# Kernel tuning notes

Measured on AMD Instinct MI355X. Metric: run time of the kernel, lower is better.

The kernel has to match this reference:

```python
import jax, jax.numpy as jnp
import numpy as np

N = 100000          # instances in the bag
L_IN = 784          # 28*28
C = 128             # size[1]
H = 2               # n_heads = len(temperature)
S = C // H          # step = 64
D = S // 2          # per-head hidden dim ('small') = 32
TEMP = jnp.array([1.0, 1.0], dtype=jnp.float32)  # temperature per head


def setup_inputs() -> dict:
    key = jax.random.key(0)
    ks = jax.random.split(key, 8)
    h = jax.random.normal(ks[0], (N, L_IN), dtype=jnp.float32)
    # shared FC: Linear(784, 128) (xavier-normal-ish init, zero bias)
    W0 = jax.random.normal(ks[1], (L_IN, C), dtype=jnp.float32) * (2.0 / (L_IN + C)) ** 0.5
    b0 = jnp.zeros((C,), dtype=jnp.float32)
    # per-head gated attention nets, stacked over head axis
    Wa = jax.random.normal(ks[2], (H, S, D), dtype=jnp.float32) * (2.0 / (S + D)) ** 0.5
    ba = jnp.zeros((H, D), dtype=jnp.float32)
    Wb = jax.random.normal(ks[3], (H, S, D), dtype=jnp.float32) * (2.0 / (S + D)) ** 0.5
    bb = jnp.zeros((H, D), dtype=jnp.float32)
    Wc = jax.random.normal(ks[4], (H, D, 1), dtype=jnp.float32) * (2.0 / (D + 1)) ** 0.5
    bc = jnp.zeros((H, 1), dtype=jnp.float32)
    # bag-level classifier: Linear(128, 1)
    Wcls = jax.random.normal(ks[5], (C, 1), dtype=jnp.float32) * (2.0 / (C + 1)) ** 0.5
    bcls = jnp.zeros((1,), dtype=jnp.float32)
    return {"h": h, "W0": W0, "b0": b0, "Wa": Wa, "ba": ba,
            "Wb": Wb, "bb": bb, "Wc": Wc, "bc": bc,
            "Wcls": Wcls, "bcls": bcls}


def reference(h, W0, b0, Wa, ba, Wb, bb, Wc, bc, Wcls, bcls):
    # shared FC + ReLU: [N,784] -> [N,128]
    x = jax.nn.relu(h @ W0 + b0)
    x = x.reshape(-1, H, S)                                  # [N,H,S]
    # gated attention per head, batched over heads via einsum
    a = jnp.tanh(jnp.einsum('nhs,hsd->nhd', x, Wa) + ba)     # [N,H,D]
    g = jax.nn.sigmoid(jnp.einsum('nhs,hsd->nhd', x, Wb) + bb)
    A = (jnp.einsum('nhd,hdo->nho', a * g, Wc) + bc)[..., 0] # [N,H]
    A = A / TEMP                                             # temperature scaling per head
    Aw = jax.nn.softmax(A, axis=0)                           # softmax over instances N
    # weighted instance pooling: [1, H*S] = [1, 128]
    M = jnp.einsum('nh,nhs->hs', Aw, x).reshape(1, H * S)
    logits = (M @ Wcls + bcls)[:, 0]                         # [1]
    Y_prob = jax.nn.sigmoid(logits)
    Y_hat = (Y_prob >= 0.5).astype(jnp.float32)
    return (Y_prob, Y_hat)
```

## Files before the change

kernel.cpp:

```cpp
#include <hip/hip_runtime.h>
#include <stdint.h>
#include <math.h>

typedef unsigned short u16;
typedef unsigned int   u32;
typedef __bf16 bf16x8 __attribute__((ext_vector_type(8)));
typedef float  f32x4  __attribute__((ext_vector_type(4)));

#define L_IN 784
#define KPAD 832
#define KT_N 13

__device__ __forceinline__ u32 f2bf(float f){
    u32 u = __float_as_uint(f);
    return (u + 0x7fffu + ((u >> 16) & 1u)) >> 16;
}

__device__ __forceinline__ void gload16(const void* g, void* l){
    __builtin_amdgcn_global_load_lds(
        (const __attribute__((address_space(1))) unsigned char*)g,
        (__attribute__((address_space(3))) unsigned char*)l, 16, 0, 0);
}

__global__ void prep_w0(const float* __restrict__ W0, u16* __restrict__ Bimg){
    int idx = blockIdx.x * 256 + threadIdx.x;
    if (idx >= KPAD * 128) return;
    int j  = idx & 7;
    int l  = (idx >> 3) & 63;
    int nt = (idx >> 9) & 7;
    int kk = (idx >> 12) & 1;
    int kt = idx >> 13;
    int col = nt * 16 + (l & 15);
    int k   = kt * 64 + kk * 32 + (l >> 4) * 8 + j;
    float v = (k < L_IN) ? W0[k * 128 + col] : 0.f;
    Bimg[idx] = (u16)f2bf(v);
}

__global__ void prep_wab(const float* __restrict__ Wa, const float* __restrict__ Wb,
                         u16* __restrict__ Wab){
    int idx = blockIdx.x * 256 + threadIdx.x;
    if (idx >= 16384) return;
    int jj  = idx & 7;
    int l   = (idx >> 3) & 63;
    int ks  = (idx >> 9) & 1;
    int nt  = (idx >> 10) & 1;
    int h   = (idx >> 11) & 1;
    int mat = (idx >> 12) & 1;
    int s = ks * 32 + (l >> 4) * 8 + jj;
    int d = nt * 16 + (l & 15);
    const float* W = mat ? Wb : Wa;
    Wab[idx] = (u16)f2bf(W[h * 2048 + s * 32 + d]);
}

__global__ __launch_bounds__(256, 4)
void fc_fused(const float* __restrict__ hG, const u16* __restrict__ Bimg,
              const u16* __restrict__ Wab, const float* __restrict__ b0,
              const float* __restrict__ ba, const float* __restrict__ bb,
              const float* __restrict__ Wc, const float* __restrict__ bc,
              float* __restrict__ partials, int N){
    __shared__ __align__(16) float As[2][64 * 64];

    const int t    = threadIdx.x;
    const int lane = t & 63;
    const int w    = t >> 6;
    const int lr   = lane & 15;
    const int lk   = lane >> 4;
    const int gb   = blockIdx.x;
    const long rowBase = (long)gb * 64;

    const int rloc = t >> 4;
    const int csw  = (t & 15) ^ ((rloc & 3) << 1);
    const float* srcp[4];
    #pragma unroll
    for (int j = 0; j < 4; ++j){
        long grow = rowBase + j * 16 + rloc;
        if (grow >= N) grow = N - 1;
        srcp[j] = hG + grow * L_IN + csw * 4;
    }

    f32x4 acc[8];
    #pragma unroll
    for (int nt = 0; nt < 8; ++nt) acc[nt] = (f32x4)0.f;

    auto stage = [&](int kt, int buf){
        #pragma unroll
        for (int j = 0; j < 4; ++j){
            const float* src = (kt == KT_N - 1 && csw >= 4)
                             ? (srcp[j] - csw * 4)
                             : (srcp[j] + kt * 64);
            gload16(src, (char*)&As[buf][0] + (j * 256 + t) * 16);
        }
    };

    stage(0, 0);
    int cur = 0;
    const int rA = w * 16 + lr;

    #pragma unroll 1
    for (int kt = 0; kt < KT_N; ++kt){
        __syncthreads();

        const u16* bp = Bimg + (size_t)(kt * 2) * 4096 + lane * 8;
        bf16x8 b0f[8], b1f[8];
        #pragma unroll
        for (int nt = 0; nt < 8; ++nt)
            b0f[nt] = *(const bf16x8*)(bp + nt * 512);
        #pragma unroll
        for (int nt = 0; nt < 8; ++nt)
            b1f[nt] = *(const bf16x8*)(bp + 4096 + nt * 512);
        __builtin_amdgcn_sched_barrier(0);

        if (kt + 1 < KT_N) stage(kt + 1, cur ^ 1);
        __builtin_amdgcn_sched_barrier(0);

        #pragma unroll
        for (int kk = 0; kk < 2; ++kk){
            const int q = kk * 4 + (lk ^ (rA & 3));
            f32x4 lo = *(const f32x4*)&As[cur][rA * 64 + q * 8];
            f32x4 hi = *(const f32x4*)&As[cur][rA * 64 + q * 8 + 4];
            bf16x8 af;
            #pragma unroll
            for (int j = 0; j < 4; ++j){
                af[j]     = (__bf16)lo[j];
                af[4 + j] = (__bf16)hi[j];
            }
            #pragma unroll
            for (int nt = 0; nt < 8; ++nt)
                acc[nt] = __builtin_amdgcn_mfma_f32_16x16x32_bf16(
                              af, kk ? b1f[nt] : b0f[nt], acc[nt], 0, 0, 0);
        }
        cur ^= 1;
    }

    __syncthreads();

    u16*   xs   = (u16*)&As[0][0];
    float* pbuf = &As[1][0];
    #pragma unroll
    for (int nt = 0; nt < 8; ++nt){
        float bias = b0[nt * 16 + lr];
        #pragma unroll
        for (int j = 0; j < 4; ++j){
            float v = acc[nt][j] + bias;
            v = v > 0.f ? v : 0.f;
            acc[nt][j] = v;
            int row = w * 16 + lk * 4 + j;
            int col = nt * 16 + lr;
            xs[row * 128 + ((((col >> 3) ^ (row & 15))) << 3) + (col & 7)] = (u16)f2bf(v);
        }
    }
    __syncthreads();

    float eh[2][4];
    #pragma unroll
    for (int h = 0; h < 2; ++h){
        bf16x8 xa[2];
        #pragma unroll
        for (int ks = 0; ks < 2; ++ks){
            int row = w * 16 + lr;
            int ch  = (h * 8 + ks * 4 + lk) ^ (row & 15);
            xa[ks] = *(const bf16x8*)&xs[row * 128 + ch * 8];
        }
        f32x4 Ca[2], Cg[2];
        #pragma unroll
        for (int nt = 0; nt < 2; ++nt){ Ca[nt] = (f32x4)0.f; Cg[nt] = (f32x4)0.f; }
        #pragma unroll
        for (int nt = 0; nt < 2; ++nt)
            #pragma unroll
            for (int ks = 0; ks < 2; ++ks){
                bf16x8 wfa = *(const bf16x8*)(Wab + ((size_t)(h*4 + nt*2 + ks) << 9) + lane * 8);
                bf16x8 wfb = *(const bf16x8*)(Wab + ((size_t)(8 + h*4 + nt*2 + ks) << 9) + lane * 8);
                Ca[nt] = __builtin_amdgcn_mfma_f32_16x16x32_bf16(xa[ks], wfa, Ca[nt], 0, 0, 0);
                Cg[nt] = __builtin_amdgcn_mfma_f32_16x16x32_bf16(xa[ks], wfb, Cg[nt], 0, 0, 0);
            }
        float pj[4];
        #pragma unroll
        for (int j = 0; j < 4; ++j){
            float s = 0.f;
            #pragma unroll
            for (int nt = 0; nt < 2; ++nt){
                int d = h * 32 + nt * 16 + lr;
                float av = tanhf(Ca[nt][j] + ba[d]);
                float gv = 1.f / (1.f + expf(-(Cg[nt][j] + bb[d])));
                s += av * gv * Wc[d];
            }
            pj[j] = s;
        }
        #pragma unroll
        for (int m = 1; m <= 8; m <<= 1)
            #pragma unroll
            for (int j = 0; j < 4; ++j)
                pj[j] += __shfl_xor(pj[j], m, 64);
        #pragma unroll
        for (int j = 0; j < 4; ++j){
            long row = rowBase + w * 16 + lk * 4 + j;
            eh[h][j] = (row < (long)N) ? expf(pj[j] + bc[h]) : 0.f;
        }
    }

    float p[8];
    #pragma unroll
    for (int nt = 0; nt < 8; ++nt){
        const int h = nt >> 2;
        float s = 0.f;
        #pragma unroll
        for (int j = 0; j < 4; ++j) s += eh[h][j] * acc[nt][j];
        p[nt] = s;
    }
    #pragma unroll
    for (int m = 16; m <= 32; m <<= 1)
        #pragma unroll
        for (int nt = 0; nt < 8; ++nt)
            p[nt] += __shfl_xor(p[nt], m, 64);
    float es0 = eh[0][0] + eh[0][1] + eh[0][2] + eh[0][3];
    float es1 = eh[1][0] + eh[1][1] + eh[1][2] + eh[1][3];
    es0 += __shfl_xor(es0, 16, 64); es0 += __shfl_xor(es0, 32, 64);
    es1 += __shfl_xor(es1, 16, 64); es1 += __shfl_xor(es1, 32, 64);

    if (lk == 0){
        #pragma unroll
        for (int nt = 0; nt < 8; ++nt)
            pbuf[w * 132 + nt * 16 + lr] = p[nt];
    }
    if (lane == 0){
        pbuf[w * 132 + 128] = es0;
        pbuf[w * 132 + 129] = es1;
    }
    __syncthreads();
    if (t < 130){
        float s = pbuf[t] + pbuf[132 + t] + pbuf[264 + t] + pbuf[396 + t];
        partials[(size_t)gb * 132 + t] = s;
    }
}

__global__ __launch_bounds__(256)
void reduce1(const float* __restrict__ partials, float* __restrict__ red, int nb){
    const int b = blockIdx.x, t = threadIdx.x;
    if (t >= 130) return;
    float a = 0.f;
    for (int r = b; r < nb; r += 128)
        a += partials[(size_t)r * 132 + t];
    red[b * 132 + t] = a;
}

__global__ __launch_bounds__(256)
void finalize2(const float* __restrict__ red, const float* __restrict__ Wcls,
               const float* __restrict__ bcls, float* __restrict__ out){
    __shared__ double colD[130];
    __shared__ float  M_s[128];
    const int t = threadIdx.x;
    if (t < 130){
        double s = 0.0;
        for (int r = 0; r < 128; ++r) s += (double)red[r * 132 + t];
        colD[t] = s;
    }
    __syncthreads();
    if (t < 128)
        M_s[t] = (float)(colD[t] / colD[128 + (t >> 6)]);
    __syncthreads();
    if (t == 0){
        double lg = (double)bcls[0];
        for (int c = 0; c < 128; ++c) lg += (double)M_s[c] * (double)Wcls[c];
        float pr = (float)(1.0 / (1.0 + exp(-lg)));
        out[0] = pr;
        out[1] = (lg >= 0.0) ? 1.f : 0.f;
    }
}

extern "C" void kernel_launch(void* const* d_in, const int* in_sizes, int n_in,
                              void* d_out, int out_size, void* d_ws, size_t ws_size,
                              hipStream_t stream){
    const float* hG   = (const float*)d_in[0];
    const float* W0   = (const float*)d_in[1];
    const float* b0   = (const float*)d_in[2];
    const float* Wa   = (const float*)d_in[3];
    const float* ba   = (const float*)d_in[4];
    const float* Wb   = (const float*)d_in[5];
    const float* bb   = (const float*)d_in[6];
    const float* Wc   = (const float*)d_in[7];
    const float* bc   = (const float*)d_in[8];
    const float* Wcls = (const float*)d_in[9];
    const float* bcls = (const float*)d_in[10];

    const int N    = in_sizes[0] / L_IN;
    const int nb64 = (N + 63) / 64;

    char* ws = (char*)d_ws;
    u16* Bimg = (u16*)ws;
    u16* Wab  = (u16*)(ws + 262144);
    size_t poff = 262144 + 16384;
    float* partials = (float*)(ws + poff);
    size_t roff = poff + (((size_t)nb64 * 132 * 4 + 4095) & ~(size_t)4095);
    float* red  = (float*)(ws + roff);

    prep_w0  <<<(KPAD * 128 + 255) / 256, 256, 0, stream>>>(W0, Bimg);
    prep_wab <<<64, 256, 0, stream>>>(Wa, Wb, Wab);
    fc_fused <<<nb64, 256, 0, stream>>>(hG, Bimg, Wab, b0, ba, bb, Wc, bc,
                                        partials, N);
    reduce1  <<<128, 256, 0, stream>>>(partials, red, nb64);
    finalize2<<<1, 256, 0, stream>>>(red, Wcls, bcls, (float*)d_out);
}
```

Measured before the change: 121.3 us.

## Triple-buffer the h tile loads and trim the small prep and reduce kernels

The main fc kernel moves from double to triple buffering of the fp32 input tiles in LDS. Loads are now issued two k-steps ahead, and later iterations use a raw s_barrier instead of __syncthreads. Occupancy drops from 4 to 3 blocks per CU to fit the larger LDS footprint. The two weight-prep kernels are merged into one launch, the W0 repack now reads W0 coalesced, and reduce1 and finalize2 get more parallelism and ILP. Relying on a bare barrier with asynchronous global-to-LDS loads risks reading stale data if the needed wait counts are not emitted, and lower occupancy may reduce latency hiding.

Result: faster. 115.3 us (-4.9%).

```diff
diff --git a/kernel.cpp b/kernel.cpp
--- a/kernel.cpp
+++ b/kernel.cpp
@@ -22,43 +22,33 @@
         (__attribute__((address_space(3))) unsigned char*)l, 16, 0, 0);
 }
 
-__global__ void prep_w0(const float* __restrict__ W0, u16* __restrict__ Bimg){
-    int idx = blockIdx.x * 256 + threadIdx.x;
-    if (idx >= KPAD * 128) return;
-    int j  = idx & 7;
-    int l  = (idx >> 3) & 63;
-    int nt = (idx >> 9) & 7;
-    int kk = (idx >> 12) & 1;
-    int kt = idx >> 13;
-    int col = nt * 16 + (l & 15);
-    int k   = kt * 64 + kk * 32 + (l >> 4) * 8 + j;
-    float v = (k < L_IN) ? W0[k * 128 + col] : 0.f;
-    Bimg[idx] = (u16)f2bf(v);
-}
-
-__global__ void prep_wab(const float* __restrict__ Wa, const float* __restrict__ Wb,
+__global__ void prep_all(const float* __restrict__ W0, const float* __restrict__ Wa,
+                         const float* __restrict__ Wb, u16* __restrict__ Bimg,
                          u16* __restrict__ Wab){
     int idx = blockIdx.x * 256 + threadIdx.x;
-    if (idx >= 16384) return;
-    int jj  = idx & 7;
-    int l   = (idx >> 3) & 63;
-    int ks  = (idx >> 9) & 1;
-    int nt  = (idx >> 10) & 1;
-    int h   = (idx >> 11) & 1;
-    int mat = (idx >> 12) & 1;
-    int s = ks * 32 + (l >> 4) * 8 + jj;
-    int d = nt * 16 + (l & 15);
-    const float* W = mat ? Wb : Wa;
-    Wab[idx] = (u16)f2bf(W[h * 2048 + s * 32 + d]);
-}
-
-__global__ __launch_bounds__(256, 4)
+    if (idx < KPAD * 128){
+        int col = idx & 127, k = idx >> 7;
+        float v = (k < L_IN) ? W0[idx] : 0.f;
+        int kt = k >> 6, kk = (k >> 5) & 1, j = k & 7, sl = (k >> 3) & 3;
+        Bimg[(((kt * 2 + kk) * 8 + (col >> 4)) << 9) + (sl * 16 + (col & 15)) * 8 + j]
+            = (u16)f2bf(v);
+    } else if (idx < KPAD * 128 + 16384){
+        int i2 = idx - KPAD * 128;
+        int jj = i2 & 7, l = (i2 >> 3) & 63, ks = (i2 >> 9) & 1;
+        int nt = (i2 >> 10) & 1, h = (i2 >> 11) & 1, mat = (i2 >> 12) & 1;
+        int s = ks * 32 + (l >> 4) * 8 + jj, d = nt * 16 + (l & 15);
+        const float* W = mat ? Wb : Wa;
+        Wab[i2] = (u16)f2bf(W[h * 2048 + s * 32 + d]);
+    }
+}
+
+__global__ __launch_bounds__(256, 3)
 void fc_fused(const float* __restrict__ hG, const u16* __restrict__ Bimg,
               const u16* __restrict__ Wab, const float* __restrict__ b0,
               const float* __restrict__ ba, const float* __restrict__ bb,
               const float* __restrict__ Wc, const float* __restrict__ bc,
               float* __restrict__ partials, int N){
-    __shared__ __align__(16) float As[2][64 * 64];
+    __shared__ __align__(16) char Asm[3 * 16384];
 
     const int t    = threadIdx.x;
     const int lane = t & 63;
@@ -82,23 +72,29 @@
     #pragma unroll
     for (int nt = 0; nt < 8; ++nt) acc[nt] = (f32x4)0.f;
 
-    auto stage = [&](int kt, int buf){
+    auto stage = [&](int kt, char* regn){
         #pragma unroll
         for (int j = 0; j < 4; ++j){
             const float* src = (kt == KT_N - 1 && csw >= 4)
                              ? (srcp[j] - csw * 4)
                              : (srcp[j] + kt * 64);
-            gload16(src, (char*)&As[buf][0] + (j * 256 + t) * 16);
+            gload16(src, regn + (j * 256 + t) * 16);
         }
     };
 
-    stage(0, 0);
-    int cur = 0;
+    char* p0 = &Asm[0];
+    char* p1 = &Asm[16384];
+    char* p2 = &Asm[32768];
+    stage(0, p0);
+    stage(1, p1);
+
     const int rA = w * 16 + lr;
 
     #pragma unroll 1
     for (int kt = 0; kt < KT_N; ++kt){
-        __syncthreads();
+        if (kt == 0) __syncthreads();
+        else         __builtin_amdgcn_s_barrier();
+        __builtin_amdgcn_sched_barrier(0);
 
         const u16* bp = Bimg + (size_t)(kt * 2) * 4096 + lane * 8;
         bf16x8 b0f[8], b1f[8];
@@ -110,14 +106,14 @@
             b1f[nt] = *(const bf16x8*)(bp + 4096 + nt * 512);
         __builtin_amdgcn_sched_barrier(0);
 
-        if (kt + 1 < KT_N) stage(kt + 1, cur ^ 1);
+        if (kt + 2 < KT_N) stage(kt + 2, p2);
         __builtin_amdgcn_sched_barrier(0);
 
         #pragma unroll
         for (int kk = 0; kk < 2; ++kk){
             const int q = kk * 4 + (lk ^ (rA & 3));
-            f32x4 lo = *(const f32x4*)&As[cur][rA * 64 + q * 8];
-            f32x4 hi = *(const f32x4*)&As[cur][rA * 64 + q * 8 + 4];
+            f32x4 lo = *(const f32x4*)(p0 + (rA * 64 + q * 8) * 4);
+            f32x4 hi = *(const f32x4*)(p0 + (rA * 64 + q * 8 + 4) * 4);
             bf16x8 af;
             #pragma unroll
             for (int j = 0; j < 4; ++j){
@@ -129,13 +125,13 @@
                 acc[nt] = __builtin_amdgcn_mfma_f32_16x16x32_bf16(
                               af, kk ? b1f[nt] : b0f[nt], acc[nt], 0, 0, 0);
         }
-        cur ^= 1;
-    }
-
-    __syncthreads();
-
-    u16*   xs   = (u16*)&As[0][0];
-    float* pbuf = &As[1][0];
+        char* tmp = p0; p0 = p1; p1 = p2; p2 = tmp;
+    }
+
+    __syncthreads();
+
+    u16*   xs   = (u16*)&Asm[0];
+    float* pbuf = (float*)&Asm[16384];
     #pragma unroll
     for (int nt = 0; nt < 8; ++nt){
         float bias = b0[nt * 16 + lr];
@@ -237,33 +233,53 @@
 void reduce1(const float* __restrict__ partials, float* __restrict__ red, int nb){
     const int b = blockIdx.x, t = threadIdx.x;
     if (t >= 130) return;
-    float a = 0.f;
-    for (int r = b; r < nb; r += 128)
-        a += partials[(size_t)r * 132 + t];
-    red[b * 132 + t] = a;
+    float a0 = 0.f, a1 = 0.f;
+    for (int r = b; r < nb; r += 256){
+        a0 += partials[(size_t)r * 132 + t];
+        if (r + 128 < nb) a1 += partials[(size_t)(r + 128) * 132 + t];
+    }
+    red[b * 132 + t] = a0 + a1;
 }
 
 __global__ __launch_bounds__(256)
 void finalize2(const float* __restrict__ red, const float* __restrict__ Wcls,
                const float* __restrict__ bcls, float* __restrict__ out){
-    __shared__ double colD[130];
+    __shared__ double colD[2][130];
     __shared__ float  M_s[128];
     const int t = threadIdx.x;
-    if (t < 130){
+    const int c = t & 127, rh = t >> 7;
+    {
         double s = 0.0;
-        for (int r = 0; r < 128; ++r) s += (double)red[r * 132 + t];
-        colD[t] = s;
+        for (int r = rh * 64; r < rh * 64 + 64; r += 4){
+            s += (double)red[(r + 0) * 132 + c] + (double)red[(r + 1) * 132 + c]
+               + (double)red[(r + 2) * 132 + c] + (double)red[(r + 3) * 132 + c];
+        }
+        colD[rh][c] = s;
+    }
+    if (t < 4){
+        int cc = 128 + (t & 1), hh = t >> 1;
+        double s = 0.0;
+        for (int r = hh * 64; r < hh * 64 + 64; r += 4){
+            s += (double)red[(r + 0) * 132 + cc] + (double)red[(r + 1) * 132 + cc]
+               + (double)red[(r + 2) * 132 + cc] + (double)red[(r + 3) * 132 + cc];
+        }
+        colD[hh][cc] = s;
     }
     __syncthreads();
     if (t < 128)
-        M_s[t] = (float)(colD[t] / colD[128 + (t >> 6)]);
-    __syncthreads();
-    if (t == 0){
-        double lg = (double)bcls[0];
-        for (int c = 0; c < 128; ++c) lg += (double)M_s[c] * (double)Wcls[c];
-        float pr = (float)(1.0 / (1.0 + exp(-lg)));
-        out[0] = pr;
-        out[1] = (lg >= 0.0) ? 1.f : 0.f;
+        M_s[t] = (float)((colD[0][t] + colD[1][t]) /
+                         (colD[0][128 + (t >> 6)] + colD[1][128 + (t >> 6)]));
+    __syncthreads();
+    if (t < 64){
+        double d = (double)M_s[t] * (double)Wcls[t]
+                 + (double)M_s[t + 64] * (double)Wcls[t + 64];
+        #pragma unroll
+        for (int m = 1; m < 64; m <<= 1) d += __shfl_xor(d, m, 64);
+        if (t == 0){
+            double lg = d + (double)bcls[0];
+            out[0] = (float)(1.0 / (1.0 + exp(-lg)));
+            out[1] = (lg >= 0.0) ? 1.f : 0.f;
+        }
     }
 }
 
@@ -293,8 +309,7 @@
     size_t roff = poff + (((size_t)nb64 * 132 * 4 + 4095) & ~(size_t)4095);
     float* red  = (float*)(ws + roff);
 
-    prep_w0  <<<(KPAD * 128 + 255) / 256, 256, 0, stream>>>(W0, Bimg);
-    prep_wab <<<64, 256, 0, stream>>>(Wa, Wb, Wab);
+    prep_all <<<(KPAD * 128 + 16384 + 255) / 256, 256, 0, stream>>>(W0, Wa, Wb, Bimg, Wab);
     fc_fused <<<nb64, 256, 0, stream>>>(hG, Bimg, Wab, b0, ba, bb, Wc, bc,
                                         partials, N);
     reduce1  <<<128, 256, 0, stream>>>(partials, red, nb64);
```
